# Kernel tuning notes

Measured on AMD Instinct MI355X. Metric: run time of the kernel, lower is better.

## Reference

```python
import jax, jax.numpy as jnp
import numpy as np

EMBED = 1024
HEADS = 16
HEAD_DIM = EMBED // HEADS
NEG = -1e20


def setup_inputs() -> dict:
    key = jax.random.key(0)
    ks = jax.random.split(key, 12)
    N, S, E = 2, 2048, EMBED
    w = lambda k: (jax.random.normal(k, (E, E), dtype=jnp.float32) * 0.02)
    b = lambda k: (jax.random.normal(k, (E,), dtype=jnp.float32) * 0.02)
    return {
        "values": jax.random.normal(ks[0], (N, S, E), dtype=jnp.float32),
        "keys": jax.random.normal(ks[1], (N, S, E), dtype=jnp.float32),
        "query": jax.random.normal(ks[2], (N, S, E), dtype=jnp.float32),
        "mask": jnp.ones((N, S), dtype=jnp.int32),
        "Wv": w(ks[3]), "bv": b(ks[4]),
        "Wk": w(ks[5]), "bk": b(ks[6]),
        "Wq": w(ks[7]), "bq": b(ks[8]),
        "Wo": w(ks[9]), "bo": b(ks[10]),
    }


def reference(values, keys, query, mask, Wv, bv, Wk, bk, Wq, bq, Wo, bo):
    N, S, E = query.shape
    # torch nn.Linear: x @ W.T + b
    v = (values @ Wv.T + bv).reshape(N, S, HEADS, HEAD_DIM)
    k = (keys @ Wk.T + bk).reshape(N, S, HEADS, HEAD_DIM)
    q = (query @ Wq.T + bq).reshape(N, S, HEADS, HEAD_DIM)
    # full [N,H,Q,K] score matrix, as in the original einsum
    energy = jnp.einsum('nqhd,nkhd->nhqk', q, k)
    # 2D mask with mismatched dims triggers causal tril path in the original
    causal = jnp.tril(jnp.ones((S, S), dtype=bool))  # [Q,K]
    energy = jnp.where(causal[None, None, :, :], energy, NEG)
    # NOTE: original scales by sqrt(embed_size), not sqrt(head_dim)
    attn = jax.nn.softmax(energy / jnp.sqrt(jnp.float32(E)), axis=3)
    out = jnp.einsum('nhqk,nkhd->nqhd', attn, v).reshape(N, S, E)
    return out @ Wo.T + bo
```

## Files before the change

kernel.cpp:

```cpp
#include <hip/hip_runtime.h>

typedef __bf16 bf16;
typedef __bf16 bf16x4 __attribute__((ext_vector_type(4)));
typedef __bf16 bf16x8 __attribute__((ext_vector_type(8)));
typedef float floatx4 __attribute__((ext_vector_type(4)));

#define GLOAD_LDS16(gp, lp) \
  __builtin_amdgcn_global_load_lds( \
      (const __attribute__((address_space(1))) void*)(gp), \
      (__attribute__((address_space(3))) void*)(lp), 16, 0, 0)

__global__ __launch_bounds__(256) void cvt_all_kernel(
    const float* __restrict__ v, const float* __restrict__ k, const float* __restrict__ q,
    const float* __restrict__ wv, const float* __restrict__ wk,
    const float* __restrict__ wq, const float* __restrict__ wo,
    bf16* __restrict__ xv, bf16* __restrict__ xk, bf16* __restrict__ xq,
    bf16* __restrict__ bwv, bf16* __restrict__ bwk, bf16* __restrict__ bwq,
    bf16* __restrict__ bwo) {
  const int i = blockIdx.x * 256 + threadIdx.x;
  const int A4 = 1 << 20;
  const float* src; bf16* dst; int off;
  if (i < A4)            { src = v; dst = xv; off = i; }
  else if (i < 2 * A4)   { src = k; dst = xk; off = i - A4; }
  else if (i < 3 * A4)   { src = q; dst = xq; off = i - 2 * A4; }
  else {
    int j = i - 3 * A4; int r = j >> 18; off = j & ((1 << 18) - 1);
    src = (r == 0) ? wv : (r == 1) ? wk : (r == 2) ? wq : wo;
    dst = (r == 0) ? bwv : (r == 1) ? bwk : (r == 2) ? bwq : bwo;
  }
  float4 x = reinterpret_cast<const float4*>(src)[off];
  union { bf16 b[4]; short4 s; } u;
  u.b[0] = (bf16)x.x; u.b[1] = (bf16)x.y; u.b[2] = (bf16)x.z; u.b[3] = (bf16)x.w;
  reinterpret_cast<short4*>(dst)[off] = u.s;
}

template <int MODE>
__device__ __forceinline__ void gemm_body(
    const bf16* __restrict__ A, const bf16* __restrict__ B,
    const float* __restrict__ bias, void* __restrict__ Cout,
    int bx, int by, bf16* __restrict__ SMEM) {
  constexpr int K = 1024;
  constexpr int NSTEP = K / 32;
  const int tid = threadIdx.x;
  const int lane = tid & 63;
  const int wave = tid >> 6;
  const int quad = lane >> 4;
  const int l16 = lane & 15;
  const int wm = (wave >> 1) * 64;
  const int wn = (wave & 1) * 64;
  const int am0 = by * 128;
  const int bn0 = bx * 128;
  const int srow = lane >> 2;
  const int scol = (lane & 3) * 8;

  floatx4 acc[4][4] = {};

  auto stage = [&](int step, int bufsel) {
    const int k0 = step * 32;
    bf16* As = SMEM + bufsel * 8192;
    bf16* Bs = As + 4096;
#pragma unroll
    for (int j = 0; j < 2; j++) {
      const int chunk = wave * 2 + j;
      const int row = chunk * 16 + srow;
      GLOAD_LDS16(A + (size_t)(am0 + row) * K + k0 + scol, As + chunk * 512);
      GLOAD_LDS16(B + (size_t)(bn0 + row) * K + k0 + scol, Bs + chunk * 512);
    }
  };

  auto compute = [&](int bufsel) {
    const bf16* As = SMEM + bufsel * 8192;
    const bf16* Bs = As + 4096;
    bf16x8 af[4], bfv[4];
#pragma unroll
    for (int mi = 0; mi < 4; mi++)
      af[mi] = *reinterpret_cast<const bf16x8*>(&As[(wm + mi * 16 + l16) * 32 + quad * 8]);
#pragma unroll
    for (int ni = 0; ni < 4; ni++)
      bfv[ni] = *reinterpret_cast<const bf16x8*>(&Bs[(wn + ni * 16 + l16) * 32 + quad * 8]);
#pragma unroll
    for (int mi = 0; mi < 4; mi++)
#pragma unroll
      for (int ni = 0; ni < 4; ni++)
        acc[mi][ni] = __builtin_amdgcn_mfma_f32_16x16x32_bf16(af[mi], bfv[ni], acc[mi][ni], 0, 0, 0);
  };

  stage(0, 0);
  for (int t = 0; t < NSTEP; t += 2) {
    __syncthreads();
    stage(t + 1, 1);
    compute(0);
    __syncthreads();
    if (t + 2 < NSTEP) stage(t + 2, 0);
    compute(1);
  }

  __syncthreads();
  bf16* T = SMEM + wave * 2048;
  const int nb = (am0 + wm) >> 11;
  const int sq0 = (am0 + wm) & 2047;
  const int h = (bn0 + wn) >> 6;
  const int nh = nb * 16 + h;
  const int r8 = lane >> 3, c8 = lane & 7;

  if constexpr (MODE == 0) {
#pragma unroll
    for (int pp = 0; pp < 2; pp++) {
#pragma unroll
      for (int mm = 0; mm < 2; mm++) {
        const int mi = pp * 2 + mm;
#pragma unroll
        for (int ni = 0; ni < 4; ni++) {
          const int d = ni * 16 + l16;
          const float bc = bias[bn0 + wn + d];
#pragma unroll
          for (int r = 0; r < 4; r++) {
            const int s = mm * 16 + quad * 4 + r;
            T[s * 64 + (d & 7) + 8 * ((d >> 3) ^ (s & 7))] = (bf16)(acc[mi][ni][r] + bc);
          }
        }
      }
#pragma unroll
      for (int it = 0; it < 4; it++) {
        const int s = it * 8 + r8;
        bf16x8 vv = *reinterpret_cast<const bf16x8*>(&T[s * 64 + ((c8 ^ r8) * 8)]);
        *reinterpret_cast<bf16x8*>(
            reinterpret_cast<bf16*>(Cout) +
            ((size_t)nh * 2048 + sq0 + pp * 32 + s) * 64 + c8 * 8) = vv;
      }
    }
  } else {
#pragma unroll
    for (int pp = 0; pp < 2; pp++) {
#pragma unroll
      for (int nn = 0; nn < 2; nn++) {
        const int ni = pp * 2 + nn;
        const int dp = nn * 16 + l16;
        const float bc = bias[bn0 + wn + pp * 32 + dp];
#pragma unroll
        for (int mi = 0; mi < 4; mi++) {
#pragma unroll
          for (int r = 0; r < 4; r++) {
            const int s = mi * 16 + quad * 4 + r;
            T[dp * 64 + (s & 7) + 8 * ((s >> 3) ^ (dp & 7))] = (bf16)(acc[mi][ni][r] + bc);
          }
        }
      }
#pragma unroll
      for (int it = 0; it < 4; it++) {
        const int dp = it * 8 + r8;
        bf16x8 vv = *reinterpret_cast<const bf16x8*>(&T[dp * 64 + ((c8 ^ r8) * 8)]);
        *reinterpret_cast<bf16x8*>(
            reinterpret_cast<bf16*>(Cout) +
            ((size_t)nh * 64 + pp * 32 + dp) * 2048 + sq0 + c8 * 8) = vv;
      }
    }
  }
}

__global__ __launch_bounds__(256) void gemm_qkv(
    const bf16* __restrict__ A0, const bf16* __restrict__ B0, const float* __restrict__ c0, bf16* __restrict__ C0,
    const bf16* __restrict__ A1, const bf16* __restrict__ B1, const float* __restrict__ c1, bf16* __restrict__ C1,
    const bf16* __restrict__ A2, const bf16* __restrict__ B2, const float* __restrict__ c2, bf16* __restrict__ C2) {
  extern __shared__ __align__(16) bf16 SMEM[];
  const int lin = blockIdx.x + (blockIdx.y << 3) + (blockIdx.z << 8);
  const int swz = (lin & 7) * 96 + (lin >> 3);
  const int bz = swz >> 8;
  const int by = (swz >> 3) & 31;
  const int bx = swz & 7;
  if (bz == 0)      gemm_body<0>(A0, B0, c0, C0, bx, by, SMEM);
  else if (bz == 1) gemm_body<0>(A1, B1, c1, C1, bx, by, SMEM);
  else              gemm_body<1>(A2, B2, c2, C2, bx, by, SMEM);
}

__global__ __launch_bounds__(256) void gemm_out(
    const bf16* __restrict__ A, const bf16* __restrict__ B,
    const float* __restrict__ bias, float* __restrict__ C) {
  extern __shared__ __align__(16) bf16 SMEM[];
  constexpr int K = 1024, N = 1024;
  constexpr int NSTEP = 32;
  const int lin = blockIdx.x + (blockIdx.y << 4);
  const int swz = (lin & 7) * 64 + (lin >> 3);
  const int by = swz >> 4;
  const int bx = swz & 15;
  const int tid = threadIdx.x;
  const int lane = tid & 63;
  const int wave = tid >> 6;
  const int quad = lane >> 4;
  const int l16 = lane & 15;
  const int wm = (wave >> 1) * 64;
  const int wn = (wave & 1) * 32;
  const int am0 = by * 128;
  const int bn0 = bx * 64;
  const int srow = lane >> 2;
  const int scol = (lane & 3) * 8;

  floatx4 acc[4][2] = {};

  auto stage = [&](int step, int bufsel) {
    const int k0 = step * 32;
    bf16* As = SMEM + bufsel * 6144;
    bf16* Bs = As + 4096;
#pragma unroll
    for (int j = 0; j < 2; j++) {
      const int chunk = wave * 2 + j;
      const int row = chunk * 16 + srow;
      GLOAD_LDS16(A + (size_t)(am0 + row) * K + k0 + scol, As + chunk * 512);
    }
    {
      const int row = wave * 16 + srow;
      GLOAD_LDS16(B + (size_t)(bn0 + row) * K + k0 + scol, Bs + wave * 512);
    }
  };

  auto compute = [&](int bufsel) {
    const bf16* As = SMEM + bufsel * 6144;
    const bf16* Bs = As + 4096;
    bf16x8 af[4], bfv[2];
#pragma unroll
    for (int mi = 0; mi < 4; mi++)
      af[mi] = *reinterpret_cast<const bf16x8*>(&As[(wm + mi * 16 + l16) * 32 + quad * 8]);
#pragma unroll
    for (int ni = 0; ni < 2; ni++)
      bfv[ni] = *reinterpret_cast<const bf16x8*>(&Bs[(wn + ni * 16 + l16) * 32 + quad * 8]);
#pragma unroll
    for (int mi = 0; mi < 4; mi++)
#pragma unroll
      for (int ni = 0; ni < 2; ni++)
        acc[mi][ni] = __builtin_amdgcn_mfma_f32_16x16x32_bf16(af[mi], bfv[ni], acc[mi][ni], 0, 0, 0);
  };

  stage(0, 0);
  for (int t = 0; t < NSTEP; t += 2) {
    __syncthreads();
    stage(t + 1, 1);
    compute(0);
    __syncthreads();
    if (t + 2 < NSTEP) stage(t + 2, 0);
    compute(1);
  }

#pragma unroll
  for (int mi = 0; mi < 4; mi++) {
#pragma unroll
    for (int ni = 0; ni < 2; ni++) {
      const int col = bn0 + wn + ni * 16 + l16;
      const float bb = bias[col];
      const int row = am0 + wm + mi * 16 + quad * 4;
#pragma unroll
      for (int r = 0; r < 4; r++)
        C[(size_t)(row + r) * N + col] = acc[mi][ni][r] + bb;
    }
  }
}

#define S_LEN 2048
#define EMB 1024
#define QT 128
#define KTILE 64
#define SCALE2 (0.03125f * 1.44269504f)

__global__ __launch_bounds__(256) void attn_kernel(
    const bf16* __restrict__ Qh, const bf16* __restrict__ Kh,
    const bf16* __restrict__ Vt, bf16* __restrict__ O,
    float* __restrict__ Opart, float* __restrict__ lpart) {
  __shared__ __align__(16) bf16 Ks[2 * KTILE * 64];
  __shared__ __align__(16) bf16 Vs[2 * 64 * KTILE];

  const int tid = threadIdx.x;
  const int lane = tid & 63;
  const int wave = tid >> 6;
  const int quad = lane >> 4;
  const int l16 = lane & 15;
  const int wq = wave * 32;

  const int c = blockIdx.x;
  const int role = blockIdx.y;
  const int nh = c >> 3;
  const int t = c & 7;
  const int n = nh >> 4;
  const int h = nh & 15;
  int qt, kt0, kt1;
  if (role == 0) { qt = t; kt0 = 0; kt1 = 2 * t + 2; }
  else {
    qt = 15 - t;
    const int halfk = qt + 1;
    kt0 = (role == 1) ? 0 : halfk;
    kt1 = (role == 1) ? halfk : 2 * halfk;
  }
  const int q0 = qt * QT;

  bf16x8 aq[2][2];
  {
    const bf16* Qb = Qh + ((size_t)nh * S_LEN + q0 + wq + l16) * 64 + quad * 8;
#pragma unroll
    for (int mi = 0; mi < 2; mi++)
#pragma unroll
      for (int kc = 0; kc < 2; kc++)
        aq[mi][kc] = *reinterpret_cast<const bf16x8*>(Qb + mi * 16 * 64 + kc * 32);
  }

  float l_part[2] = {};
  floatx4 o_acc[2][4] = {};

  const bf16* Kbase = Kh + (size_t)nh * S_LEN * 64;
  const bf16* Vbase = Vt + (size_t)nh * 64 * S_LEN;

  const int srl = lane >> 3;
  const int sc8 = lane & 7;

  auto stage = [&](int kt) {
    const int k0s = kt * KTILE;
    const int buf = (kt & 1) * 4096;
#pragma unroll
    for (int j = 0; j < 2; j++) {
      const int rl = wave * 16 + j * 8 + srl;
      const int c8s = ((sc8 ^ (rl & 7)) * 8);
      GLOAD_LDS16(Kbase + (size_t)(k0s + rl) * 64 + c8s, Ks + buf + (wave * 16 + j * 8) * 64);
      GLOAD_LDS16(Vbase + (size_t)rl * S_LEN + k0s + c8s, Vs + buf + (wave * 16 + j * 8) * 64);
    }
  };

  stage(kt0);
  for (int kt = kt0; kt < kt1; kt++) {
    const int k0 = kt * KTILE;
    __syncthreads();
    if (kt + 1 < kt1) stage(kt + 1);
    const bf16* Kc = Ks + (kt & 1) * 4096;
    const bf16* Vc = Vs + (kt & 1) * 4096;

    floatx4 s_acc[2][4] = {};
#pragma unroll
    for (int kc = 0; kc < 2; kc++) {
      bf16x8 bk[4];
#pragma unroll
      for (int ni = 0; ni < 4; ni++)
        bk[ni] = *reinterpret_cast<const bf16x8*>(
            &Kc[(ni * 16 + l16) * 64 + (((kc * 4 + quad) ^ (l16 & 7)) * 8)]);
#pragma unroll
      for (int mi = 0; mi < 2; mi++)
#pragma unroll
        for (int ni = 0; ni < 4; ni++)
          s_acc[mi][ni] = __builtin_amdgcn_mfma_f32_16x16x32_bf16(bk[ni], aq[mi][kc], s_acc[mi][ni], 0, 0, 0);
    }

    const bool needMask = (k0 + KTILE - 1) > (q0 + wq);
    const int qg = q0 + wq + l16;
    union PU { bf16x8 w[2]; bf16x4 q[4]; };
    PU P[2];
#pragma unroll
    for (int mi = 0; mi < 2; mi++) {
#pragma unroll
      for (int ni = 0; ni < 4; ni++) {
        const int kgb = k0 + ni * 16 + quad * 4;
        bf16x4 pk;
#pragma unroll
        for (int r = 0; r < 4; r++) {
          float pr = __builtin_amdgcn_exp2f(s_acc[mi][ni][r] * SCALE2);
          if (needMask) pr = ((kgb + r) <= (qg + mi * 16)) ? pr : 0.f;
          l_part[mi] += pr;
          pk[r] = (bf16)pr;
        }
        P[mi].q[ni] = pk;
      }
    }

#pragma unroll
    for (int kc = 0; kc < 2; kc++) {
      bf16x8 bv[4];
#pragma unroll
      for (int di = 0; di < 4; di++) {
        const bf16* base = Vc + (di * 16 + l16) * 64;
        const int e = l16 & 7;
        union VU { bf16x8 v8; bf16x4 h[2]; } vu;
        vu.h[0] = *reinterpret_cast<const bf16x4*>(
            base + (((kc * 4 + (quad >> 1)) ^ e) * 8) + (quad & 1) * 4);
        vu.h[1] = *reinterpret_cast<const bf16x4*>(
            base + (((kc * 4 + 2 + (quad >> 1)) ^ e) * 8) + (quad & 1) * 4);
        bv[di] = vu.v8;
      }
#pragma unroll
      for (int mi = 0; mi < 2; mi++)
#pragma unroll
        for (int di = 0; di < 4; di++)
          o_acc[mi][di] = __builtin_amdgcn_mfma_f32_16x16x32_bf16(P[mi].w[kc], bv[di], o_acc[mi][di], 0, 0, 0);
    }
  }

  float l_sum[2];
#pragma unroll
  for (int mi = 0; mi < 2; mi++) {
    float s = l_part[mi];
    s += __shfl_xor(s, 16);
    s += __shfl_xor(s, 32);
    l_sum[mi] = s;
  }

  if (role == 0) {
    bf16* Op = O + ((size_t)(n * S_LEN + q0 + wq)) * EMB + h * 64;
#pragma unroll
    for (int mi = 0; mi < 2; mi++) {
      const float linv = 1.0f / l_sum[mi];
#pragma unroll
      for (int r = 0; r < 4; r++) {
        const float inv = __shfl(linv, quad * 4 + r);
        bf16* orow = Op + (size_t)(mi * 16 + quad * 4 + r) * EMB;
#pragma unroll
        for (int di = 0; di < 4; di++)
          orow[di * 16 + l16] = (bf16)(o_acc[mi][di][r] * inv);
      }
    }
  } else {
    float* Ob = Opart + ((size_t)c * 2 + (role - 1)) * (QT * 64);
    float* lb = lpart + ((size_t)c * 2 + (role - 1)) * QT;
#pragma unroll
    for (int mi = 0; mi < 2; mi++)
      if (lane < 16) lb[wq + mi * 16 + lane] = l_sum[mi];
#pragma unroll
    for (int mi = 0; mi < 2; mi++)
#pragma unroll
      for (int r = 0; r < 4; r++) {
        float* orow = Ob + (size_t)(wq + mi * 16 + quad * 4 + r) * 64;
#pragma unroll
        for (int di = 0; di < 4; di++)
          orow[di * 16 + l16] = o_acc[mi][di][r];
      }
  }
}

__global__ __launch_bounds__(256) void attn_combine(
    const float* __restrict__ Opart, const float* __restrict__ lpart,
    bf16* __restrict__ O) {
  const int c = blockIdx.x;
  const int nh = c >> 3;
  const int t = c & 7;
  const int qt = 15 - t;
  const int n = nh >> 4;
  const int h = nh & 15;
  const float* O1 = Opart + (size_t)c * 2 * (QT * 64);
  const float* O2 = O1 + QT * 64;
  const float* l1 = lpart + (size_t)c * 2 * QT;
  const float* l2 = l1 + QT;
  const int tid = threadIdx.x;
  for (int i = tid; i < QT * 64 / 4; i += 256) {
    const int row = i >> 4;
    const float inv = 1.0f / (l1[row] + l2[row]);
    float4 a = reinterpret_cast<const float4*>(O1)[i];
    float4 b = reinterpret_cast<const float4*>(O2)[i];
    bf16x4 pk;
    pk[0] = (bf16)((a.x + b.x) * inv);
    pk[1] = (bf16)((a.y + b.y) * inv);
    pk[2] = (bf16)((a.z + b.z) * inv);
    pk[3] = (bf16)((a.w + b.w) * inv);
    *reinterpret_cast<bf16x4*>(
        O + ((size_t)(n * S_LEN + qt * QT + row)) * EMB + h * 64 + (i & 15) * 4) = pk;
  }
}

extern "C" void kernel_launch(void* const* d_in, const int* in_sizes, int n_in,
                              void* d_out, int out_size, void* d_ws, size_t ws_size,
                              hipStream_t stream) {
  (void)in_sizes; (void)n_in; (void)out_size; (void)ws_size;
  const float* values = (const float*)d_in[0];
  const float* keys   = (const float*)d_in[1];
  const float* query  = (const float*)d_in[2];
  const float* Wv = (const float*)d_in[4];
  const float* bv = (const float*)d_in[5];
  const float* Wk = (const float*)d_in[6];
  const float* bk = (const float*)d_in[7];
  const float* Wq = (const float*)d_in[8];
  const float* bq = (const float*)d_in[9];
  const float* Wo = (const float*)d_in[10];
  const float* bo = (const float*)d_in[11];
  float* out = (float*)d_out;

  const int S = 2048, E = 1024;
  const int M = 2 * S;
  const size_t MB_ = 1u << 20;
  char* ws = (char*)d_ws;
  bf16* xv  = (bf16*)(ws + 0 * MB_);
  bf16* xk  = (bf16*)(ws + 8 * MB_);
  bf16* xq  = (bf16*)(ws + 16 * MB_);
  bf16* wvb = (bf16*)(ws + 24 * MB_);
  bf16* wkb = (bf16*)(ws + 26 * MB_);
  bf16* wqb = (bf16*)(ws + 28 * MB_);
  bf16* wob = (bf16*)(ws + 30 * MB_);
  bf16* kh  = (bf16*)(ws + 32 * MB_);
  bf16* qh  = (bf16*)(ws + 40 * MB_);
  bf16* vt  = (bf16*)(ws + 48 * MB_);
  bf16* ao  = (bf16*)(ws + 56 * MB_);
  float* Opart = (float*)(ws + 0 * MB_);
  float* lpart = (float*)(ws + 17 * MB_);

  cvt_all_kernel<<<(4 << 20) / 256, 256, 0, stream>>>(
      values, keys, query, Wv, Wk, Wq, Wo,
      xv, xk, xq, wvb, wkb, wqb, wob);

  gemm_qkv<<<dim3(E / 128, M / 128, 3), 256, 32768, stream>>>(
      xq, wqb, bq, qh,
      xk, wkb, bk, kh,
      xv, wvb, bv, vt);

  attn_kernel<<<dim3(256, 3), 256, 0, stream>>>(qh, kh, vt, ao, Opart, lpart);
  attn_combine<<<dim3(256), 256, 0, stream>>>(Opart, lpart, ao);

  gemm_out<<<dim3(16, 32), 256, 24576, stream>>>(ao, wob, bo, out);
}
```

Measured before the change: 220.9 us.

## Fuse fp32-to-bf16 conversion into GEMM operand loads, drop conversion kernel

```diff
diff --git a/kernel.cpp b/kernel.cpp
--- a/kernel.cpp
+++ b/kernel.cpp
@@ -10,34 +10,10 @@
       (const __attribute__((address_space(1))) void*)(gp), \
       (__attribute__((address_space(3))) void*)(lp), 16, 0, 0)
 
-__global__ __launch_bounds__(256) void cvt_all_kernel(
-    const float* __restrict__ v, const float* __restrict__ k, const float* __restrict__ q,
-    const float* __restrict__ wv, const float* __restrict__ wk,
-    const float* __restrict__ wq, const float* __restrict__ wo,
-    bf16* __restrict__ xv, bf16* __restrict__ xk, bf16* __restrict__ xq,
-    bf16* __restrict__ bwv, bf16* __restrict__ bwk, bf16* __restrict__ bwq,
-    bf16* __restrict__ bwo) {
-  const int i = blockIdx.x * 256 + threadIdx.x;
-  const int A4 = 1 << 20;
-  const float* src; bf16* dst; int off;
-  if (i < A4)            { src = v; dst = xv; off = i; }
-  else if (i < 2 * A4)   { src = k; dst = xk; off = i - A4; }
-  else if (i < 3 * A4)   { src = q; dst = xq; off = i - 2 * A4; }
-  else {
-    int j = i - 3 * A4; int r = j >> 18; off = j & ((1 << 18) - 1);
-    src = (r == 0) ? wv : (r == 1) ? wk : (r == 2) ? wq : wo;
-    dst = (r == 0) ? bwv : (r == 1) ? bwk : (r == 2) ? bwq : bwo;
-  }
-  float4 x = reinterpret_cast<const float4*>(src)[off];
-  union { bf16 b[4]; short4 s; } u;
-  u.b[0] = (bf16)x.x; u.b[1] = (bf16)x.y; u.b[2] = (bf16)x.z; u.b[3] = (bf16)x.w;
-  reinterpret_cast<short4*>(dst)[off] = u.s;
-}
-
 template <int MODE>
 __device__ __forceinline__ void gemm_body(
-    const bf16* __restrict__ A, const bf16* __restrict__ B,
-    const float* __restrict__ bias, void* __restrict__ Cout,
+    const float* __restrict__ A, const float* __restrict__ B,
+    const float* __restrict__ bias, bf16* __restrict__ Cout,
     int bx, int by, bf16* __restrict__ SMEM) {
   constexpr int K = 1024;
   constexpr int NSTEP = K / 32;
@@ -54,17 +30,34 @@
   const int scol = (lane & 3) * 8;
 
   floatx4 acc[4][4] = {};
-
-  auto stage = [&](int step, int bufsel) {
+  float4 ra[2][2], rb[2][2];
+
+  auto loadRegs = [&](int step) {
     const int k0 = step * 32;
+#pragma unroll
+    for (int j = 0; j < 2; j++) {
+      const int row = (wave * 2 + j) * 16 + srow;
+      const float* pa = A + (size_t)(am0 + row) * K + k0 + scol;
+      ra[j][0] = *reinterpret_cast<const float4*>(pa);
+      ra[j][1] = *reinterpret_cast<const float4*>(pa + 4);
+      const float* pb = B + (size_t)(bn0 + row) * K + k0 + scol;
+      rb[j][0] = *reinterpret_cast<const float4*>(pb);
+      rb[j][1] = *reinterpret_cast<const float4*>(pb + 4);
+    }
+  };
+
+  auto cvtWrite = [&](int bufsel) {
     bf16* As = SMEM + bufsel * 8192;
     bf16* Bs = As + 4096;
 #pragma unroll
     for (int j = 0; j < 2; j++) {
-      const int chunk = wave * 2 + j;
-      const int row = chunk * 16 + srow;
-      GLOAD_LDS16(A + (size_t)(am0 + row) * K + k0 + scol, As + chunk * 512);
-      GLOAD_LDS16(B + (size_t)(bn0 + row) * K + k0 + scol, Bs + chunk * 512);
+      const int off = (wave * 2 + j) * 512 + lane * 8;
+      bf16x8 va = {(bf16)ra[j][0].x, (bf16)ra[j][0].y, (bf16)ra[j][0].z, (bf16)ra[j][0].w,
+                   (bf16)ra[j][1].x, (bf16)ra[j][1].y, (bf16)ra[j][1].z, (bf16)ra[j][1].w};
+      bf16x8 vb = {(bf16)rb[j][0].x, (bf16)rb[j][0].y, (bf16)rb[j][0].z, (bf16)rb[j][0].w,
+                   (bf16)rb[j][1].x, (bf16)rb[j][1].y, (bf16)rb[j][1].z, (bf16)rb[j][1].w};
+      *reinterpret_cast<bf16x8*>(As + off) = va;
+      *reinterpret_cast<bf16x8*>(Bs + off) = vb;
     }
   };
 
@@ -85,14 +78,17 @@
         acc[mi][ni] = __builtin_amdgcn_mfma_f32_16x16x32_bf16(af[mi], bfv[ni], acc[mi][ni], 0, 0, 0);
   };
 
-  stage(0, 0);
+  loadRegs(0);
+  cvtWrite(0);
   for (int t = 0; t < NSTEP; t += 2) {
     __syncthreads();
-    stage(t + 1, 1);
+    loadRegs(t + 1);
     compute(0);
+    cvtWrite(1);
     __syncthreads();
-    if (t + 2 < NSTEP) stage(t + 2, 0);
+    if (t + 2 < NSTEP) loadRegs(t + 2);
     compute(1);
+    if (t + 2 < NSTEP) cvtWrite(0);
   }
 
   __syncthreads();
@@ -125,8 +121,7 @@
         const int s = it * 8 + r8;
         bf16x8 vv = *reinterpret_cast<const bf16x8*>(&T[s * 64 + ((c8 ^ r8) * 8)]);
         *reinterpret_cast<bf16x8*>(
-            reinterpret_cast<bf16*>(Cout) +
-            ((size_t)nh * 2048 + sq0 + pp * 32 + s) * 64 + c8 * 8) = vv;
+            Cout + ((size_t)nh * 2048 + sq0 + pp * 32 + s) * 64 + c8 * 8) = vv;
       }
     }
   } else {
@@ -151,17 +146,16 @@
         const int dp = it * 8 + r8;
         bf16x8 vv = *reinterpret_cast<const bf16x8*>(&T[dp * 64 + ((c8 ^ r8) * 8)]);
         *reinterpret_cast<bf16x8*>(
-            reinterpret_cast<bf16*>(Cout) +
-            ((size_t)nh * 64 + pp * 32 + dp) * 2048 + sq0 + c8 * 8) = vv;
+            Cout + ((size_t)nh * 64 + pp * 32 + dp) * 2048 + sq0 + c8 * 8) = vv;
       }
     }
   }
 }
 
 __global__ __launch_bounds__(256) void gemm_qkv(
-    const bf16* __restrict__ A0, const bf16* __restrict__ B0, const float* __restrict__ c0, bf16* __restrict__ C0,
-    const bf16* __restrict__ A1, const bf16* __restrict__ B1, const float* __restrict__ c1, bf16* __restrict__ C1,
-    const bf16* __restrict__ A2, const bf16* __restrict__ B2, const float* __restrict__ c2, bf16* __restrict__ C2) {
+    const float* __restrict__ A0, const float* __restrict__ B0, const float* __restrict__ c0, bf16* __restrict__ C0,
+    const float* __restrict__ A1, const float* __restrict__ B1, const float* __restrict__ c1, bf16* __restrict__ C1,
+    const float* __restrict__ A2, const float* __restrict__ B2, const float* __restrict__ c2, bf16* __restrict__ C2) {
   extern __shared__ __align__(16) bf16 SMEM[];
   const int lin = blockIdx.x + (blockIdx.y << 3) + (blockIdx.z << 8);
   const int swz = (lin & 7) * 96 + (lin >> 3);
@@ -174,7 +168,7 @@
 }
 
 __global__ __launch_bounds__(256) void gemm_out(
-    const bf16* __restrict__ A, const bf16* __restrict__ B,
+    const bf16* __restrict__ A, const float* __restrict__ B,
     const float* __restrict__ bias, float* __restrict__ C) {
   extern __shared__ __align__(16) bf16 SMEM[];
   constexpr int K = 1024, N = 1024;
@@ -196,21 +190,29 @@
   const int scol = (lane & 3) * 8;
 
   floatx4 acc[4][2] = {};
-
-  auto stage = [&](int step, int bufsel) {
+  float4 rb[2];
+
+  auto stageA = [&](int step, int bufsel) {
     const int k0 = step * 32;
     bf16* As = SMEM + bufsel * 6144;
-    bf16* Bs = As + 4096;
 #pragma unroll
     for (int j = 0; j < 2; j++) {
       const int chunk = wave * 2 + j;
       const int row = chunk * 16 + srow;
       GLOAD_LDS16(A + (size_t)(am0 + row) * K + k0 + scol, As + chunk * 512);
     }
-    {
-      const int row = wave * 16 + srow;
-      GLOAD_LDS16(B + (size_t)(bn0 + row) * K + k0 + scol, Bs + wave * 512);
-    }
+  };
+  auto loadB = [&](int step) {
+    const int k0 = step * 32;
+    const float* pb = B + (size_t)(bn0 + wave * 16 + srow) * K + k0 + scol;
+    rb[0] = *reinterpret_cast<const float4*>(pb);
+    rb[1] = *reinterpret_cast<const float4*>(pb + 4);
+  };
+  auto cvtWriteB = [&](int bufsel) {
+    bf16* Bs = SMEM + bufsel * 6144 + 4096;
+    bf16x8 vb = {(bf16)rb[0].x, (bf16)rb[0].y, (bf16)rb[0].z, (bf16)rb[0].w,
+                 (bf16)rb[1].x, (bf16)rb[1].y, (bf16)rb[1].z, (bf16)rb[1].w};
+    *reinterpret_cast<bf16x8*>(Bs + wave * 512 + lane * 8) = vb;
   };
 
   auto compute = [&](int bufsel) {
@@ -230,14 +232,16 @@
         acc[mi][ni] = __builtin_amdgcn_mfma_f32_16x16x32_bf16(af[mi], bfv[ni], acc[mi][ni], 0, 0, 0);
   };
 
-  stage(0, 0);
+  stageA(0, 0); loadB(0); cvtWriteB(0);
   for (int t = 0; t < NSTEP; t += 2) {
     __syncthreads();
-    stage(t + 1, 1);
+    stageA(t + 1, 1); loadB(t + 1);
     compute(0);
+    cvtWriteB(1);
     __syncthreads();
-    if (t + 2 < NSTEP) stage(t + 2, 0);
+    if (t + 2 < NSTEP) { stageA(t + 2, 0); loadB(t + 2); }
     compute(1);
+    if (t + 2 < NSTEP) cvtWriteB(0);
   }
 
 #pragma unroll
@@ -474,17 +478,10 @@
   const float* bo = (const float*)d_in[11];
   float* out = (float*)d_out;
 
-  const int S = 2048, E = 1024;
-  const int M = 2 * S;
+  const int E = 1024;
+  const int M = 2 * 2048;
   const size_t MB_ = 1u << 20;
   char* ws = (char*)d_ws;
-  bf16* xv  = (bf16*)(ws + 0 * MB_);
-  bf16* xk  = (bf16*)(ws + 8 * MB_);
-  bf16* xq  = (bf16*)(ws + 16 * MB_);
-  bf16* wvb = (bf16*)(ws + 24 * MB_);
-  bf16* wkb = (bf16*)(ws + 26 * MB_);
-  bf16* wqb = (bf16*)(ws + 28 * MB_);
-  bf16* wob = (bf16*)(ws + 30 * MB_);
   bf16* kh  = (bf16*)(ws + 32 * MB_);
   bf16* qh  = (bf16*)(ws + 40 * MB_);
   bf16* vt  = (bf16*)(ws + 48 * MB_);
@@ -492,17 +489,13 @@
   float* Opart = (float*)(ws + 0 * MB_);
   float* lpart = (float*)(ws + 17 * MB_);
 
-  cvt_all_kernel<<<(4 << 20) / 256, 256, 0, stream>>>(
-      values, keys, query, Wv, Wk, Wq, Wo,
-      xv, xk, xq, wvb, wkb, wqb, wob);
-
   gemm_qkv<<<dim3(E / 128, M / 128, 3), 256, 32768, stream>>>(
-      xq, wqb, bq, qh,
-      xk, wkb, bk, kh,
-      xv, wvb, bv, vt);
+      query, Wq, bq, qh,
+      keys, Wk, bk, kh,
+      values, Wv, bv, vt);
 
   attn_kernel<<<dim3(256, 3), 256, 0, stream>>>(qh, kh, vt, ao, Opart, lpart);
   attn_combine<<<dim3(256), 256, 0, stream>>>(Opart, lpart, ao);
 
-  gemm_out<<<dim3(16, 32), 256, 24576, stream>>>(ao, wob, bo, out);
+  gemm_out<<<dim3(16, 32), 256, 24576, stream>>>(ao, Wo, bo, out);
 }
```

New measurement: 240.5 us. 1.09x slower.
